# Kernel optimization log

Measured on AMD Instinct MI355X. Metric: run time of the kernel, lower is better.

The kernel has to match this reference:

```python
import jax, jax.numpy as jnp
import numpy as np

OUT_FEATURES = 64  # self.out_features after list unwrapping


def setup_inputs() -> dict:
    key = jax.random.key(0)
    k1, k2, k3 = jax.random.split(key, 3)
    B, T, N, F = 1, 2, 196608, 32   # zoom 7 -> 12*4^7 HEALPix cells
    K = 9                            # HEALPix neighborhood size (cell + 8 neighbors)
    UP = 4                           # out_zoom - in_zoom = 1 -> 4 child cells
    x = jax.random.normal(k1, (B, T, N, F), dtype=jnp.float32)
    adjc = jax.random.randint(k2, (N, K), 0, N, dtype=jnp.int64)
    W = jax.random.normal(k3, (K, F, UP, OUT_FEATURES), dtype=jnp.float32) / np.sqrt(K * F)
    b = jnp.zeros((UP, OUT_FEATURES), dtype=jnp.float32)
    return {"x": x, "adjc": adjc, "W": W, "b": b}


def reference(x, adjc, W, b):
    # grid_layer.get_nh: gather neighbor features via adjacency -> [B,T,N,K,F]
    nh = x[:, :, adjc, :]
    # learned transform contracting neighborhood (K) and features (F)
    # into 4 child cells (u) x out_features (o)
    out = jnp.einsum('btnkf,kfuo->btnuo', nh, W) + b
    # x.reshape(*x.shape[:3], -1, self.out_features)
    return out.reshape(*out.shape[:3], -1, OUT_FEATURES)
```

## Files before the change

kernel.cpp:

```cpp
#include <hip/hip_runtime.h>

typedef short bf16x8 __attribute__((ext_vector_type(8)));
typedef float f32x4 __attribute__((ext_vector_type(4)));
typedef unsigned short u16;

#define NNODE 196608
#define FF 32
#define KK 9
#define COLS 256
#define KTOT 288
#define WELEMS (COLS * KTOT)

__device__ __forceinline__ u16 f2bf(float f) {
    unsigned u = __builtin_bit_cast(unsigned, f);
    return (u16)((u + 0x7fffu + ((u >> 16) & 1u)) >> 16);
}

__global__ void cvt_x(const float* __restrict__ x, u16* __restrict__ xb, int n8) {
    int i = blockIdx.x * blockDim.x + threadIdx.x;
    if (i >= n8) return;
    f32x4 v0 = *((const f32x4*)x + (size_t)i * 2);
    f32x4 v1 = *((const f32x4*)x + (size_t)i * 2 + 1);
    union { u16 h[8]; bf16x8 v; } r;
    #pragma unroll
    for (int j = 0; j < 4; ++j) r.h[j] = f2bf(v0[j]);
    #pragma unroll
    for (int j = 0; j < 4; ++j) r.h[4 + j] = f2bf(v1[j]);
    *((bf16x8*)xb + i) = r.v;
}

__global__ void cvt_w(const float* __restrict__ W, u16* __restrict__ Wt) {
    int gid = blockIdx.x * 256 + threadIdx.x;
    int c = gid / KTOT;
    int kf = gid - c * KTOT;
    Wt[gid] = f2bf(W[(size_t)kf * COLS + c]);
}

__global__ __launch_bounds__(512, 2) void updown_main(
    const u16* __restrict__ xb, const u16* __restrict__ Wt,
    const int* __restrict__ adjc, const float* __restrict__ bias,
    float* __restrict__ out)
{
    __shared__ __align__(16) u16 wlds[WELEMS];

    const int tid = threadIdx.x;

    #pragma unroll
    for (int i = 0; i < 18; ++i) {
        *(bf16x8*)(wlds + i * 4096 + tid * 8) =
            *(const bf16x8*)(Wt + i * 4096 + tid * 8);
    }

    const int w    = tid >> 6;
    const int lane = tid & 63;
    const int l15  = lane & 15;
    const int q    = lane >> 4;
    const int wr   = w >> 1;
    const int wc   = w & 1;
    const int blk  = blockIdx.x;
    const int t    = (blk >= 768) ? 1 : 0;
    const int nb   = (blk - t * 768) * 256 + wr * 64;
    const int cb   = wc * 128;
    const u16* xbt = xb + (size_t)t * NNODE * FF;

    int idxC[4], idxN[4];
    #pragma unroll
    for (int mt = 0; mt < 4; ++mt) idxC[mt] = adjc[(nb + mt * 16 + l15) * 9 + 0];
    #pragma unroll
    for (int mt = 0; mt < 4; ++mt) idxN[mt] = adjc[(nb + mt * 16 + l15) * 9 + 1];

    bf16x8 aC[4], aN[4];
    #pragma unroll
    for (int mt = 0; mt < 4; ++mt)
        aC[mt] = *(const bf16x8*)(xbt + (size_t)idxC[mt] * FF + q * 8);

    f32x4 acc[4][8];
    #pragma unroll
    for (int mt = 0; mt < 4; ++mt)
        #pragma unroll
        for (int nt = 0; nt < 8; ++nt)
            acc[mt][nt] = (f32x4){0.f, 0.f, 0.f, 0.f};

    __syncthreads();

    const u16* bbase = wlds + (cb + l15) * KTOT + q * 8;

    #pragma unroll
    for (int kk = 0; kk < 9; ++kk) {
        if (kk < 8) {
            #pragma unroll
            for (int mt = 0; mt < 4; ++mt)
                aN[mt] = *(const bf16x8*)(xbt + (size_t)idxN[mt] * FF + q * 8);
            if (kk < 7) {
                #pragma unroll
                for (int mt = 0; mt < 4; ++mt)
                    idxN[mt] = adjc[(nb + mt * 16 + l15) * 9 + (kk + 2)];
            }
        }

        bf16x8 bf[8];
        #pragma unroll
        for (int nt = 0; nt < 8; ++nt)
            bf[nt] = *(const bf16x8*)(bbase + nt * 16 * KTOT + kk * 32);

        #pragma unroll
        for (int nt = 0; nt < 8; ++nt)
            #pragma unroll
            for (int mt = 0; mt < 4; ++mt)
                acc[mt][nt] = __builtin_amdgcn_mfma_f32_16x16x32_bf16(
                    aC[mt], bf[nt], acc[mt][nt], 0, 0, 0);

        if (kk < 8) {
            #pragma unroll
            for (int mt = 0; mt < 4; ++mt) aC[mt] = aN[mt];
        }
    }

    float bb[8];
    #pragma unroll
    for (int nt = 0; nt < 8; ++nt) bb[nt] = bias[cb + nt * 16 + l15];

    const size_t rowbase = (size_t)t * NNODE + nb;
    #pragma unroll
    for (int mt = 0; mt < 4; ++mt) {
        #pragma unroll
        for (int nt = 0; nt < 8; ++nt) {
            #pragma unroll
            for (int r = 0; r < 4; ++r) {
                out[(rowbase + mt * 16 + q * 4 + r) * COLS + cb + nt * 16 + l15]
                    = acc[mt][nt][r] + bb[nt];
            }
        }
    }
}

extern "C" void kernel_launch(void* const* d_in, const int* in_sizes, int n_in,
                              void* d_out, int out_size, void* d_ws, size_t ws_size,
                              hipStream_t stream) {
    const float* x    = (const float*)d_in[0];
    const int*   adjc = (const int*)d_in[1];
    const float* W    = (const float*)d_in[2];
    const float* b    = (const float*)d_in[3];
    float* out = (float*)d_out;

    u16* xb = (u16*)d_ws;
    u16* Wt = xb + (size_t)2 * NNODE * FF;

    cvt_x<<<dim3(6144), dim3(256), 0, stream>>>(x, xb, 1572864);
    cvt_w<<<dim3(288), dim3(256), 0, stream>>>(W, Wt);
    updown_main<<<dim3(1536), dim3(512), 0, stream>>>(xb, Wt, adjc, b, out);
}
```

Baseline: 156.2 us.

## Pre-swizzle weights into MFMA fragment order and widen warp row tiles

The weight conversion kernel now writes bf16 weights in per-lane MFMA fragment order, so each lane's LDS B-fragment read is contiguous (lane*8) instead of strided by KTOT, which is meant to remove LDS bank conflicts. Warps are remapped from a 4x2 grid (64 rows x 128 cols) to a 2x4 grid (128 rows x 64 cols), so each warp gathers 8 neighbor rows per k-step and reads 4 B fragments. This halves LDS traffic per MFMA but doubles the scattered global gathers and A-register pressure per warp.

```diff
diff --git a/kernel.cpp b/kernel.cpp
--- a/kernel.cpp
+++ b/kernel.cpp
@@ -31,8 +31,14 @@
 
 __global__ void cvt_w(const float* __restrict__ W, u16* __restrict__ Wt) {
     int gid = blockIdx.x * 256 + threadIdx.x;
-    int c = gid / KTOT;
-    int kf = gid - c * KTOT;
+    int f      = gid >> 9;
+    int within = gid & 511;
+    int lane   = within >> 3;
+    int e      = within & 7;
+    int kk = f >> 4, ct = f & 15;
+    int cl = lane & 15, q = lane >> 4;
+    int c  = ct * 16 + cl;
+    int kf = kk * 32 + q * 8 + e;
     Wt[gid] = f2bf(W[(size_t)kf * COLS + c]);
 }
 
@@ -55,76 +61,78 @@
     const int lane = tid & 63;
     const int l15  = lane & 15;
     const int q    = lane >> 4;
-    const int wr   = w >> 1;
-    const int wc   = w & 1;
+    const int wr   = w >> 2;
+    const int wc   = w & 3;
     const int blk  = blockIdx.x;
     const int t    = (blk >= 768) ? 1 : 0;
-    const int nb   = (blk - t * 768) * 256 + wr * 64;
-    const int cb   = wc * 128;
+    const int nb   = (blk - t * 768) * 256 + wr * 128;
+    const int cb   = wc * 64;
     const u16* xbt = xb + (size_t)t * NNODE * FF;
 
-    int idxC[4], idxN[4];
+    int idxN[8];
+    bf16x8 aC[8];
     #pragma unroll
-    for (int mt = 0; mt < 4; ++mt) idxC[mt] = adjc[(nb + mt * 16 + l15) * 9 + 0];
+    for (int mt = 0; mt < 8; ++mt) {
+        int i0 = adjc[(size_t)(nb + mt * 16 + l15) * 9 + 0];
+        aC[mt] = *(const bf16x8*)(xbt + (size_t)i0 * FF + q * 8);
+    }
     #pragma unroll
-    for (int mt = 0; mt < 4; ++mt) idxN[mt] = adjc[(nb + mt * 16 + l15) * 9 + 1];
+    for (int mt = 0; mt < 8; ++mt)
+        idxN[mt] = adjc[(size_t)(nb + mt * 16 + l15) * 9 + 1];
 
-    bf16x8 aC[4], aN[4];
+    f32x4 acc[8][4];
     #pragma unroll
-    for (int mt = 0; mt < 4; ++mt)
-        aC[mt] = *(const bf16x8*)(xbt + (size_t)idxC[mt] * FF + q * 8);
-
-    f32x4 acc[4][8];
-    #pragma unroll
-    for (int mt = 0; mt < 4; ++mt)
+    for (int mt = 0; mt < 8; ++mt)
         #pragma unroll
-        for (int nt = 0; nt < 8; ++nt)
+        for (int nt = 0; nt < 4; ++nt)
             acc[mt][nt] = (f32x4){0.f, 0.f, 0.f, 0.f};
 
     __syncthreads();
 
-    const u16* bbase = wlds + (cb + l15) * KTOT + q * 8;
+    const u16* bb0 = wlds + (size_t)(wc * 4) * 512 + lane * 8;
 
     #pragma unroll
     for (int kk = 0; kk < 9; ++kk) {
+        bf16x8 aNv[8];
         if (kk < 8) {
             #pragma unroll
-            for (int mt = 0; mt < 4; ++mt)
-                aN[mt] = *(const bf16x8*)(xbt + (size_t)idxN[mt] * FF + q * 8);
+            for (int mt = 0; mt < 8; ++mt)
+                aNv[mt] = *(const bf16x8*)(xbt + (size_t)idxN[mt] * FF + q * 8);
             if (kk < 7) {
                 #pragma unroll
-                for (int mt = 0; mt < 4; ++mt)
-                    idxN[mt] = adjc[(nb + mt * 16 + l15) * 9 + (kk + 2)];
+                for (int mt = 0; mt < 8; ++mt)
+                    idxN[mt] = adjc[(size_t)(nb + mt * 16 + l15) * 9 + (kk + 2)];
             }
         }
 
-        bf16x8 bf[8];
+        const u16* bk = bb0 + kk * 8192;
+        bf16x8 bf[4];
         #pragma unroll
-        for (int nt = 0; nt < 8; ++nt)
-            bf[nt] = *(const bf16x8*)(bbase + nt * 16 * KTOT + kk * 32);
+        for (int nt = 0; nt < 4; ++nt)
+            bf[nt] = *(const bf16x8*)(bk + nt * 512);
 
         #pragma unroll
-        for (int nt = 0; nt < 8; ++nt)
+        for (int mt = 0; mt < 8; ++mt)
             #pragma unroll
-            for (int mt = 0; mt < 4; ++mt)
+            for (int nt = 0; nt < 4; ++nt)
                 acc[mt][nt] = __builtin_amdgcn_mfma_f32_16x16x32_bf16(
                     aC[mt], bf[nt], acc[mt][nt], 0, 0, 0);
 
         if (kk < 8) {
             #pragma unroll
-            for (int mt = 0; mt < 4; ++mt) aC[mt] = aN[mt];
+            for (int mt = 0; mt < 8; ++mt) aC[mt] = aNv[mt];
         }
     }
 
-    float bb[8];
+    float bb[4];
     #pragma unroll
-    for (int nt = 0; nt < 8; ++nt) bb[nt] = bias[cb + nt * 16 + l15];
+    for (int nt = 0; nt < 4; ++nt) bb[nt] = bias[cb + nt * 16 + l15];
 
     const size_t rowbase = (size_t)t * NNODE + nb;
     #pragma unroll
-    for (int mt = 0; mt < 4; ++mt) {
+    for (int mt = 0; mt < 8; ++mt) {
         #pragma unroll
-        for (int nt = 0; nt < 8; ++nt) {
+        for (int nt = 0; nt < 4; ++nt) {
             #pragma unroll
             for (int r = 0; r < 4; ++r) {
                 out[(rowbase + mt * 16 + q * 4 + r) * COLS + cb + nt * 16 + l15]
```

Result: slower. 210.7 us (+34.9%).

## Swizzle weight layout for conflict-free LDS fragment reads and use nontemporal output stores

Applied to the files above, without the earlier changes.

The weight conversion kernel now writes W in MFMA fragment order, so each lane reads contiguous 16-byte chunks from LDS instead of rows strided by 288 elements. The goal is to remove LDS bank conflicts on the B-operand loads. Output stores become nontemporal to reduce cache pollution from the large streaming output. The MFMA loop order is also swapped and the first gather is issued right after its index load.

```diff
diff --git a/kernel.cpp b/kernel.cpp
--- a/kernel.cpp
+++ b/kernel.cpp
@@ -31,8 +31,14 @@
 
 __global__ void cvt_w(const float* __restrict__ W, u16* __restrict__ Wt) {
     int gid = blockIdx.x * 256 + threadIdx.x;
-    int c = gid / KTOT;
-    int kf = gid - c * KTOT;
+    int f      = gid >> 9;
+    int within = gid & 511;
+    int lane   = within >> 3;
+    int e      = within & 7;
+    int kk = f >> 4, ct = f & 15;
+    int cl = lane & 15, q = lane >> 4;
+    int c  = ct * 16 + cl;
+    int kf = kk * 32 + q * 8 + e;
     Wt[gid] = f2bf(W[(size_t)kf * COLS + c]);
 }
 
@@ -63,16 +69,16 @@
     const int cb   = wc * 128;
     const u16* xbt = xb + (size_t)t * NNODE * FF;
 
-    int idxC[4], idxN[4];
+    int idxN[4];
+    bf16x8 aC[4];
     #pragma unroll
-    for (int mt = 0; mt < 4; ++mt) idxC[mt] = adjc[(nb + mt * 16 + l15) * 9 + 0];
-    #pragma unroll
-    for (int mt = 0; mt < 4; ++mt) idxN[mt] = adjc[(nb + mt * 16 + l15) * 9 + 1];
-
-    bf16x8 aC[4], aN[4];
+    for (int mt = 0; mt < 4; ++mt) {
+        int i0 = adjc[(size_t)(nb + mt * 16 + l15) * 9 + 0];
+        aC[mt] = *(const bf16x8*)(xbt + (size_t)i0 * FF + q * 8);
+    }
     #pragma unroll
     for (int mt = 0; mt < 4; ++mt)
-        aC[mt] = *(const bf16x8*)(xbt + (size_t)idxC[mt] * FF + q * 8);
+        idxN[mt] = adjc[(size_t)(nb + mt * 16 + l15) * 9 + 1];
 
     f32x4 acc[4][8];
     #pragma unroll
@@ -83,36 +89,38 @@
 
     __syncthreads();
 
-    const u16* bbase = wlds + (cb + l15) * KTOT + q * 8;
+    const u16* bb0 = wlds + (size_t)(wc * 8) * 512 + lane * 8;
 
     #pragma unroll
     for (int kk = 0; kk < 9; ++kk) {
+        bf16x8 aNv[4];
         if (kk < 8) {
             #pragma unroll
             for (int mt = 0; mt < 4; ++mt)
-                aN[mt] = *(const bf16x8*)(xbt + (size_t)idxN[mt] * FF + q * 8);
+                aNv[mt] = *(const bf16x8*)(xbt + (size_t)idxN[mt] * FF + q * 8);
             if (kk < 7) {
                 #pragma unroll
                 for (int mt = 0; mt < 4; ++mt)
-                    idxN[mt] = adjc[(nb + mt * 16 + l15) * 9 + (kk + 2)];
+                    idxN[mt] = adjc[(size_t)(nb + mt * 16 + l15) * 9 + (kk + 2)];
             }
         }
 
+        const u16* bk = bb0 + kk * 8192;
         bf16x8 bf[8];
         #pragma unroll
         for (int nt = 0; nt < 8; ++nt)
-            bf[nt] = *(const bf16x8*)(bbase + nt * 16 * KTOT + kk * 32);
+            bf[nt] = *(const bf16x8*)(bk + nt * 512);
 
         #pragma unroll
-        for (int nt = 0; nt < 8; ++nt)
+        for (int mt = 0; mt < 4; ++mt)
             #pragma unroll
-            for (int mt = 0; mt < 4; ++mt)
+            for (int nt = 0; nt < 8; ++nt)
                 acc[mt][nt] = __builtin_amdgcn_mfma_f32_16x16x32_bf16(
                     aC[mt], bf[nt], acc[mt][nt], 0, 0, 0);
 
         if (kk < 8) {
             #pragma unroll
-            for (int mt = 0; mt < 4; ++mt) aC[mt] = aN[mt];
+            for (int mt = 0; mt < 4; ++mt) aC[mt] = aNv[mt];
         }
     }
 
@@ -127,8 +135,9 @@
         for (int nt = 0; nt < 8; ++nt) {
             #pragma unroll
             for (int r = 0; r < 4; ++r) {
-                out[(rowbase + mt * 16 + q * 4 + r) * COLS + cb + nt * 16 + l15]
-                    = acc[mt][nt][r] + bb[nt];
+                __builtin_nontemporal_store(
+                    acc[mt][nt][r] + bb[nt],
+                    &out[(rowbase + mt * 16 + q * 4 + r) * COLS + cb + nt * 16 + l15]);
             }
         }
     }
```

Measured after the change: 176.0 us. 12.7% more time.
